# Kernel tuning notes

Measured on AMD Instinct MI355X. Metric: run time of the kernel, lower is better.

## Reference

```python
import jax, jax.numpy as jnp
import numpy as np

B = 32          # batch (decoding sequences)
HID = 4096      # hidden_size
NH = 32         # num query heads
NKV = 8         # num kv heads
HS = 128        # head_size
BS = 16         # paged-cache block size
MAXS = 2048     # max context length
MAXB = MAXS // BS            # blocks per sequence
NBLOCKS = B * MAXB           # total cache blocks
ROPE_BASE = 10000.0


def rope(x, pos):
    # NeoX rotate-half RoPE (offset = head_size//2, rotary_ndims = head_size).
    # x: [T, n_head, HS], pos: [T] int
    half = x.shape[-1] // 2
    inv_freq = 1.0 / (ROPE_BASE ** (jnp.arange(half, dtype=jnp.float32) * 2.0 / (2 * half)))
    freqs = pos[:, None].astype(jnp.float32) * inv_freq[None, :]   # [T, half]
    cos = jnp.cos(freqs)[:, None, :]
    sin = jnp.sin(freqs)[:, None, :]
    x1, x2 = x[..., :half], x[..., half:]
    return jnp.concatenate([x1 * cos - x2 * sin, x2 * cos + x1 * sin], axis=-1)


def setup_inputs() -> dict:
    key = jax.random.key(0)
    ks = jax.random.split(key, 8)
    hidden_states = jax.random.normal(ks[0], (B, 1, HID), jnp.float32)
    wq = jax.random.normal(ks[1], (NH * HS, HID), jnp.float32) * 0.02
    wk = jax.random.normal(ks[2], (NKV * HS, HID), jnp.float32) * 0.02
    wv = jax.random.normal(ks[3], (NKV * HS, HID), jnp.float32) * 0.02
    wo = jax.random.normal(ks[4], (NH * HS, NH * HS), jnp.float32) * 0.02
    k_cache = jax.random.normal(ks[5], (NBLOCKS, BS, NKV, HS), jnp.float32)
    v_cache = jax.random.normal(ks[6], (NBLOCKS, BS, NKV, HS), jnp.float32)
    # each sequence owns a disjoint set of MAXB blocks
    block_tables = jnp.arange(NBLOCKS, dtype=jnp.int32).reshape(B, MAXB)
    input_lengths = jax.random.randint(ks[7], (B,), 1, MAXS + 1, jnp.int32)
    position_ids = (input_lengths - 1).astype(jnp.int64)  # decode: write at last position
    last = input_lengths - 1
    slots = (block_tables[jnp.arange(B), last // BS] * BS + last % BS).astype(jnp.int32)
    return {
        "hidden_states": hidden_states, "wq": wq, "wk": wk, "wv": wv, "wo": wo,
        "k_cache": k_cache, "v_cache": v_cache, "position_ids": position_ids,
        "block_tables": block_tables, "slots": slots,
        "input_lengths": input_lengths, "max_s": MAXS,
    }


def reference(hidden_states, wq, wk, wv, wo, k_cache, v_cache,
              position_ids, block_tables, slots, input_lengths, max_s):
    bsz, q_len, hid = hidden_states.shape
    x = hidden_states.reshape(bsz * q_len, hid)
    q = (x @ wq.T).reshape(-1, NH, HS)
    k = (x @ wk.T).reshape(-1, NKV, HS)
    v = (x @ wv.T).reshape(-1, NKV, HS)
    q = rope(q, position_ids)
    k = rope(k, position_ids)
    # reshape_and_cache: scatter rope'd k and v into paged cache at slot indices
    kc = k_cache.reshape(-1, NKV, HS).at[slots].set(k)   # [NBLOCKS*BS, NKV, HS]
    vc = v_cache.reshape(-1, NKV, HS).at[slots].set(v)
    # single-query paged attention: gather per-sequence K/V via block_tables
    flat_idx = (block_tables[:, :, None] * BS
                + jnp.arange(BS, dtype=block_tables.dtype)[None, None, :]).reshape(bsz, -1)  # [B, max_s]
    keys = kc[flat_idx]    # [B, S, NKV, HS]
    vals = vc[flat_idx]    # [B, S, NKV, HS]
    groups = NH // NKV
    qg = q.reshape(bsz, NKV, groups, HS)
    scale = HS ** -0.5
    scores = jnp.einsum('bhgd,bshd->bhgs', qg, keys) * scale       # [B, NKV, G, S]
    valid = jnp.arange(max_s)[None, :] < input_lengths[:, None]    # [B, S]
    scores = jnp.where(valid[:, None, None, :], scores, -jnp.inf)
    p = jax.nn.softmax(scores, axis=-1)
    attn = jnp.einsum('bhgs,bshd->bhgd', p, vals).reshape(bsz, NH * HS)
    return (attn @ wo.T).reshape(bsz, q_len, hid)
```

## Files before the change

### kernel.cpp

```cpp
#include <hip/hip_runtime.h>
#include <math.h>


__device__ __forceinline__ void gemm_body(
    const float* __restrict__ x, const float* __restrict__ w,
    float* __restrict__ dst, int dstride, int kbase, int kcnt)
{
    __shared__ float xs[32][36];
    __shared__ float wsm[32][257];
    int t = threadIdx.x;
    float acc[4][8];
#pragma unroll
    for (int i = 0; i < 4; ++i)
#pragma unroll
        for (int j = 0; j < 8; ++j) acc[i][j] = 0.f;

    int nsub = t & 31, bsub = t >> 5;

    for (int kt = 0; kt < kcnt; kt += 32) {
        int k0 = kbase + kt;
        {
            int b = t >> 3, k4 = (t & 7) << 2;
            float4 xv = *(const float4*)(x + (size_t)b * 4096 + k0 + k4);
            *(float4*)&xs[b][k4] = xv;
        }
        {
            int k4 = (t & 7) << 2;
            int nl0 = t >> 3;
#pragma unroll
            for (int i = 0; i < 8; ++i) {
                int nl = nl0 + (i << 5);
                float4 wv = *(const float4*)(w + (size_t)nl * 4096 + k0 + k4);
                wsm[k4 + 0][nl] = wv.x;
                wsm[k4 + 1][nl] = wv.y;
                wsm[k4 + 2][nl] = wv.z;
                wsm[k4 + 3][nl] = wv.w;
            }
        }
        __syncthreads();
#pragma unroll
        for (int k = 0; k < 32; ++k) {
            float xv[4], wv[8];
#pragma unroll
            for (int j = 0; j < 4; ++j) xv[j] = xs[bsub * 4 + j][k];
#pragma unroll
            for (int j = 0; j < 8; ++j) wv[j] = wsm[k][nsub + (j << 5)];
#pragma unroll
            for (int jb = 0; jb < 4; ++jb)
#pragma unroll
                for (int jn = 0; jn < 8; ++jn)
                    acc[jb][jn] = fmaf(xv[jb], wv[jn], acc[jb][jn]);
        }
        __syncthreads();
    }
#pragma unroll
    for (int jb = 0; jb < 4; ++jb) {
        int b = bsub * 4 + jb;
#pragma unroll
        for (int jn = 0; jn < 8; ++jn)
            atomicAdd(dst + (size_t)b * dstride + nsub + (jn << 5), acc[jb][jn]);
    }
}

__global__ __launch_bounds__(256) void qkv_gemm(
    const float* __restrict__ x, const float* __restrict__ wq,
    const float* __restrict__ wk, const float* __restrict__ wv,
    float* __restrict__ qb, float* __restrict__ knb, float* __restrict__ vnb)
{
    int split = blockIdx.x & 15;
    int tile  = blockIdx.x >> 4;
    const float* w; float* dst; int dstride;
    if (tile < 16)      { w = wq + (size_t)tile * 256 * 4096;        dst = qb  + tile * 256;        dstride = 4096; }
    else if (tile < 20) { w = wk + (size_t)(tile - 16) * 256 * 4096; dst = knb + (tile - 16) * 256; dstride = 1024; }
    else                { w = wv + (size_t)(tile - 20) * 256 * 4096; dst = vnb + (tile - 20) * 256; dstride = 1024; }
    gemm_body(x, w, dst, dstride, split * 256, 256);
}

__global__ __launch_bounds__(256) void wo_gemm(
    const float* __restrict__ attn, const float* __restrict__ wo,
    float* __restrict__ out)
{
    int split = blockIdx.x & 15;
    int tile  = blockIdx.x >> 4;
    gemm_body(attn, wo + (size_t)tile * 256 * 4096, out + tile * 256, 4096, split * 256, 256);
}

__global__ void rope_kernel(float* __restrict__ qb, float* __restrict__ knb,
                            const int* __restrict__ lens)
{
    int bid = blockIdx.x;
    int b = bid / 40, r = bid % 40;
    float* row = (r < 32) ? (qb + (size_t)b * 4096 + r * 128)
                          : (knb + (size_t)b * 1024 + (r - 32) * 128);
    int d = threadIdx.x;
    float pos = (float)(lens[b] - 1);
    float inv = exp2f(-(float)d * 0.207620505930460f);
    float fr = pos * inv;
    float s, c;
    sincosf(fr, &s, &c);
    float x1 = row[d], x2 = row[d + 64];
    row[d]      = x1 * c - x2 * s;
    row[d + 64] = x2 * c + x1 * s;
}

#define MUL4(V, S) { V.x *= S; V.y *= S; V.z *= S; V.w *= S; }
#define FMA4(O, P, V) { O.x = fmaf(P, V.x, O.x); O.y = fmaf(P, V.y, O.y); \
                        O.z = fmaf(P, V.z, O.z); O.w = fmaf(P, V.w, O.w); }
#define DOT8(S, QA, QB, K0, K1) { \
    S = fmaf(QA.x, K0.x, S); S = fmaf(QA.y, K0.y, S); \
    S = fmaf(QA.z, K0.z, S); S = fmaf(QA.w, K0.w, S); \
    S = fmaf(QB.x, K1.x, S); S = fmaf(QB.y, K1.y, S); \
    S = fmaf(QB.z, K1.z, S); S = fmaf(QB.w, K1.w, S); }
#define RED16(X) { X += __shfl_xor(X, 1, 64); X += __shfl_xor(X, 2, 64); \
                   X += __shfl_xor(X, 4, 64); X += __shfl_xor(X, 8, 64); }
#define REDG_SUM(X) { X += __shfl_xor(X, 16, 64); X += __shfl_xor(X, 32, 64); }
#define REDG_MAX(X) { X = fmaxf(X, __shfl_xor(X, 16, 64)); \
                      X = fmaxf(X, __shfl_xor(X, 32, 64)); }
#define REDG_SUM4(V) { REDG_SUM(V.x) REDG_SUM(V.y) REDG_SUM(V.z) REDG_SUM(V.w) }

#define ALOADR(S, r_) { \
    int sl = ss[((r_) << 2) + g]; \
    const float* kp; const float* vp; \
    if (sl < 0) { kp = knew; vp = vnew; } \
    else { kp = kc + (size_t)sl * 1024 + hoff; vp = vc + (size_t)sl * 1024 + hoff; } \
    S##k0 = *(const float4*)(kp + isl); S##k1 = *(const float4*)(kp + isl + 4); \
    S##v0 = *(const float4*)(vp + isl); S##v1 = *(const float4*)(vp + isl + 4); }

#define OUPD(s_, m_, l_, Oa_, Ob_, V0_, V1_, vld_) { \
    if (s_ > m_) { \
        float c_ = __expf(m_ - s_); \
        l_ *= c_; MUL4(Oa_, c_) MUL4(Ob_, c_) \
        m_ = s_; \
    } \
    float pe_ = vld_ ? __expf(s_ - m_) : 0.f; \
    l_ += pe_; \
    FMA4(Oa_, pe_, V0_) FMA4(Ob_, pe_, V1_) }

#define ACOMP(S, r_) { \
    float s0 = 0.f, s1 = 0.f, s2 = 0.f, s3 = 0.f; \
    DOT8(s0, q0a, q0b, S##k0, S##k1) \
    DOT8(s1, q1a, q1b, S##k0, S##k1) \
    DOT8(s2, q2a, q2b, S##k0, S##k1) \
    DOT8(s3, q3a, q3b, S##k0, S##k1) \
    RED16(s0) RED16(s1) RED16(s2) RED16(s3) \
    int vld = (((r_) << 2) + g) < pend; \
    if (!vld) { s0 = s1 = s2 = s3 = -INFINITY; } \
    OUPD(s0, m0, l0, o0a, o0b, S##v0, S##v1, vld) \
    OUPD(s1, m1, l1, o1a, o1b, S##v0, S##v1, vld) \
    OUPD(s2, m2, l2, o2a, o2b, S##v0, S##v1, vld) \
    OUPD(s3, m3, l3, o3a, o3b, S##v0, S##v1, vld) }

__global__ __launch_bounds__(64, 1) void attn_kernel(
    const float* __restrict__ kc, const float* __restrict__ vc,
    const float* __restrict__ qb, const float* __restrict__ knb,
    const float* __restrict__ vnb,
    const int* __restrict__ btab, const int* __restrict__ lens,
    float* __restrict__ part)
{
    int bid = blockIdx.x;
    int c = bid & 15, h = (bid >> 4) & 7, b = bid >> 7;
    int len = lens[b];
    int p0 = c << 7;
    if (p0 >= len) return;
    int pend = min(len - p0, 128);
    int nr = (pend + 3) >> 2;
    int last = len - 1;

    __shared__ int ss[128];

    int lane = threadIdx.x;
    int g = lane >> 4;
    int isl = (lane & 15) << 3;
    int hoff = h * 128;

    {
        int idx = lane << 1;
        int p = p0 + idx;
        int bt = btab[b * 128 + (p >> 4)];
        int base = bt * 16 + (p & 15);
        ss[idx]     = (p     == last) ? -1 : base;
        ss[idx + 1] = (p + 1 == last) ? -1 : base + 1;
    }

    const float* knew = knb + ((size_t)b * 8 + h) * 128;
    const float* vnew = vnb + ((size_t)b * 8 + h) * 128;

    const float scale = 0.08838834764831845f;
    const float* qrow = qb + (size_t)b * 4096 + (size_t)h * 512;
    float4 q0a = *(const float4*)(qrow + isl),       q0b = *(const float4*)(qrow + isl + 4);
    float4 q1a = *(const float4*)(qrow + 128 + isl), q1b = *(const float4*)(qrow + 128 + isl + 4);
    float4 q2a = *(const float4*)(qrow + 256 + isl), q2b = *(const float4*)(qrow + 256 + isl + 4);
    float4 q3a = *(const float4*)(qrow + 384 + isl), q3b = *(const float4*)(qrow + 384 + isl + 4);
    MUL4(q0a, scale) MUL4(q0b, scale) MUL4(q1a, scale) MUL4(q1b, scale)
    MUL4(q2a, scale) MUL4(q2b, scale) MUL4(q3a, scale) MUL4(q3b, scale)

    float m0 = -INFINITY, m1 = -INFINITY, m2 = -INFINITY, m3 = -INFINITY;
    float l0 = 0.f, l1 = 0.f, l2 = 0.f, l3 = 0.f;
    float4 o0a = {0,0,0,0}, o0b = {0,0,0,0}, o1a = {0,0,0,0}, o1b = {0,0,0,0};
    float4 o2a = {0,0,0,0}, o2b = {0,0,0,0}, o3a = {0,0,0,0}, o3b = {0,0,0,0};

    float4 ak0, ak1, av0, av1;
    float4 bk0, bk1, bv0, bv1;
    float4 ck0, ck1, cv0, cv1;
    ALOADR(a, 0)
    if (1 < nr) ALOADR(b, 1)
    if (2 < nr) ALOADR(c, 2)
    for (int r = 0; r < nr; r += 3) {
        ACOMP(a, r)
        if (r + 3 < nr) ALOADR(a, r + 3)
        if (r + 1 >= nr) break;
        ACOMP(b, r + 1)
        if (r + 4 < nr) ALOADR(b, r + 4)
        if (r + 2 >= nr) break;
        ACOMP(c, r + 2)
        if (r + 5 < nr) ALOADR(c, r + 5)
    }

    float M0 = m0, M1 = m1, M2 = m2, M3 = m3;
    REDG_MAX(M0) REDG_MAX(M1) REDG_MAX(M2) REDG_MAX(M3)
    float w0 = __expf(m0 - M0), w1 = __expf(m1 - M1);
    float w2 = __expf(m2 - M2), w3 = __expf(m3 - M3);
    float L0 = w0 * l0, L1 = w1 * l1, L2 = w2 * l2, L3 = w3 * l3;
    REDG_SUM(L0) REDG_SUM(L1) REDG_SUM(L2) REDG_SUM(L3)
    MUL4(o0a, w0) MUL4(o0b, w0) MUL4(o1a, w1) MUL4(o1b, w1)
    MUL4(o2a, w2) MUL4(o2b, w2) MUL4(o3a, w3) MUL4(o3b, w3)
    REDG_SUM4(o0a) REDG_SUM4(o0b) REDG_SUM4(o1a) REDG_SUM4(o1b)
    REDG_SUM4(o2a) REDG_SUM4(o2b) REDG_SUM4(o3a) REDG_SUM4(o3b)

    float* pgb = part + (size_t)(((b * 8 + h) * 16 + c) * 4) * 132;
    if (lane < 16) {
        *(float4*)(pgb +       isl) = o0a; *(float4*)(pgb +       isl + 4) = o0b;
        *(float4*)(pgb + 132 + isl) = o1a; *(float4*)(pgb + 132 + isl + 4) = o1b;
        *(float4*)(pgb + 264 + isl) = o2a; *(float4*)(pgb + 264 + isl + 4) = o2b;
        *(float4*)(pgb + 396 + isl) = o3a; *(float4*)(pgb + 396 + isl + 4) = o3b;
    }
    if (lane == 0) {
        pgb[128] = M0; pgb[129] = L0;
        pgb[260] = M1; pgb[261] = L1;
        pgb[392] = M2; pgb[393] = L2;
        pgb[524] = M3; pgb[525] = L3;
    }
}

__global__ __launch_bounds__(256) void combine_kernel(
    const float* __restrict__ part, const int* __restrict__ lens,
    float* __restrict__ attn)
{
    int b = blockIdx.x >> 3, h = blockIdx.x & 7;
    int t = threadIdx.x;
    int g = t >> 6, lane = t & 63;
    int len = lens[b];
    int nch = (len + 127) >> 7;
    const float* base = part + (size_t)(b * 8 + h) * 8448 + (size_t)g * 132;
    float M = -INFINITY;
    for (int cc = 0; cc < nch; ++cc)
        M = fmaxf(M, base[(size_t)cc * 528 + 128]);
    float denom = 0.f, a0 = 0.f, a1 = 0.f;
    int d0 = lane << 1;
    for (int cc = 0; cc < nch; ++cc) {
        const float* pg = base + (size_t)cc * 528;
        float w = __expf(pg[128] - M);
        denom += w * pg[129];
        a0 += w * pg[d0];
        a1 += w * pg[d0 + 1];
    }
    float inv = 1.f / denom;
    float* dst = attn + (size_t)b * 4096 + (size_t)(h * 4 + g) * 128 + d0;
    dst[0] = a0 * inv;
    dst[1] = a1 * inv;
}

extern "C" void kernel_launch(void* const* d_in, const int* in_sizes, int n_in,
                              void* d_out, int out_size, void* d_ws, size_t ws_size,
                              hipStream_t stream)
{
    const float* x   = (const float*)d_in[0];
    const float* wq  = (const float*)d_in[1];
    const float* wk  = (const float*)d_in[2];
    const float* wv  = (const float*)d_in[3];
    const float* wo  = (const float*)d_in[4];
    const float* kc  = (const float*)d_in[5];
    const float* vc  = (const float*)d_in[6];
    const int* btab  = (const int*)d_in[8];
    const int* lens  = (const int*)d_in[10];

    float* qb   = (float*)d_ws;
    float* knb  = qb  + 32 * 4096;
    float* vnb  = knb + 32 * 1024;
    float* attn = vnb + 32 * 1024;
    float* part = attn + 32 * 4096;
    float* outp = (float*)d_out;

    hipMemsetAsync(d_ws, 0, (size_t)(32 * 4096 + 2 * 32 * 1024) * sizeof(float), stream);
    hipMemsetAsync(d_out, 0, (size_t)32 * 4096 * sizeof(float), stream);

    qkv_gemm<<<24 * 16, 256, 0, stream>>>(x, wq, wk, wv, qb, knb, vnb);
    rope_kernel<<<32 * 40, 64, 0, stream>>>(qb, knb, lens);
    attn_kernel<<<4096, 64, 0, stream>>>(kc, vc, qb, knb, vnb, btab, lens, part);
    combine_kernel<<<256, 256, 0, stream>>>(part, lens, attn);
    wo_gemm<<<16 * 16, 256, 0, stream>>>(attn, wo, outp);
}
```

Before: 178.1 us.

## Remap attention so each wave covers all KV heads over 32-token chunks

Restructures the paged attention kernel so a 64-lane wave handles one batch and a 32-token chunk across all 8 KV heads. Each 8-lane group owns one head, and each lane holds 16 contiguous dims. Every token row of the K/V cache is therefore read as one contiguous 4 KB span instead of 512-byte per-head slices. The change also drops the shared-memory slot table and the cross-group softmax reduction, and shortens the shuffle reduction to 8 lanes. In exchange the kernel uses more registers per lane, has no inner validity masking, and produces four times more partial chunks for the combine kernel to merge.

After: 199.0 us. +11.7%, slower.

```diff
diff --git a/kernel.cpp b/kernel.cpp
--- a/kernel.cpp
+++ b/kernel.cpp
@@ -103,52 +103,50 @@
     row[d + 64] = x2 * c + x1 * s;
 }
 
-#define MUL4(V, S) { V.x *= S; V.y *= S; V.z *= S; V.w *= S; }
-#define FMA4(O, P, V) { O.x = fmaf(P, V.x, O.x); O.y = fmaf(P, V.y, O.y); \
-                        O.z = fmaf(P, V.z, O.z); O.w = fmaf(P, V.w, O.w); }
-#define DOT8(S, QA, QB, K0, K1) { \
-    S = fmaf(QA.x, K0.x, S); S = fmaf(QA.y, K0.y, S); \
-    S = fmaf(QA.z, K0.z, S); S = fmaf(QA.w, K0.w, S); \
-    S = fmaf(QB.x, K1.x, S); S = fmaf(QB.y, K1.y, S); \
-    S = fmaf(QB.z, K1.z, S); S = fmaf(QB.w, K1.w, S); }
-#define RED16(X) { X += __shfl_xor(X, 1, 64); X += __shfl_xor(X, 2, 64); \
-                   X += __shfl_xor(X, 4, 64); X += __shfl_xor(X, 8, 64); }
-#define REDG_SUM(X) { X += __shfl_xor(X, 16, 64); X += __shfl_xor(X, 32, 64); }
-#define REDG_MAX(X) { X = fmaxf(X, __shfl_xor(X, 16, 64)); \
-                      X = fmaxf(X, __shfl_xor(X, 32, 64)); }
-#define REDG_SUM4(V) { REDG_SUM(V.x) REDG_SUM(V.y) REDG_SUM(V.z) REDG_SUM(V.w) }
-
-#define ALOADR(S, r_) { \
-    int sl = ss[((r_) << 2) + g]; \
-    const float* kp; const float* vp; \
-    if (sl < 0) { kp = knew; vp = vnew; } \
-    else { kp = kc + (size_t)sl * 1024 + hoff; vp = vc + (size_t)sl * 1024 + hoff; } \
-    S##k0 = *(const float4*)(kp + isl); S##k1 = *(const float4*)(kp + isl + 4); \
-    S##v0 = *(const float4*)(vp + isl); S##v1 = *(const float4*)(vp + isl + 4); }
-
-#define OUPD(s_, m_, l_, Oa_, Ob_, V0_, V1_, vld_) { \
+#define V4MUL(V, S) { V.x *= S; V.y *= S; V.z *= S; V.w *= S; }
+#define V4FMA(O, P, V) { O.x = fmaf(P, V.x, O.x); O.y = fmaf(P, V.y, O.y); \
+                         O.z = fmaf(P, V.z, O.z); O.w = fmaf(P, V.w, O.w); }
+#define DOT4(S, Q, K) { S = fmaf(Q.x, K.x, S); S = fmaf(Q.y, K.y, S); \
+                        S = fmaf(Q.z, K.z, S); S = fmaf(Q.w, K.w, S); }
+#define RED8(X) { X += __shfl_xor(X, 1, 64); X += __shfl_xor(X, 2, 64); \
+                  X += __shfl_xor(X, 4, 64); }
+
+#define LOADR(S, r_) { \
+    int p_ = p0 + (r_); \
+    const float* kp_; const float* vp_; \
+    if (p_ == last) { kp_ = knew; vp_ = vnew; } \
+    else { \
+        int sl_ = ((r_) < 16) ? (bt0x16 + (r_)) : (bt1x16 + (r_) - 16); \
+        kp_ = kc + (size_t)sl_ * 1024 + l16; \
+        vp_ = vc + (size_t)sl_ * 1024 + l16; \
+    } \
+    S##k0 = *(const float4*)(kp_);      S##k1 = *(const float4*)(kp_ + 4); \
+    S##k2 = *(const float4*)(kp_ + 8);  S##k3 = *(const float4*)(kp_ + 12); \
+    S##v0 = *(const float4*)(vp_);      S##v1 = *(const float4*)(vp_ + 4); \
+    S##v2 = *(const float4*)(vp_ + 8);  S##v3 = *(const float4*)(vp_ + 12); }
+
+#define OUPD(S, s_, m_, l_, O0_, O1_, O2_, O3_) { \
     if (s_ > m_) { \
         float c_ = __expf(m_ - s_); \
-        l_ *= c_; MUL4(Oa_, c_) MUL4(Ob_, c_) \
+        l_ *= c_; V4MUL(O0_, c_) V4MUL(O1_, c_) V4MUL(O2_, c_) V4MUL(O3_, c_) \
         m_ = s_; \
     } \
-    float pe_ = vld_ ? __expf(s_ - m_) : 0.f; \
+    float pe_ = __expf(s_ - m_); \
     l_ += pe_; \
-    FMA4(Oa_, pe_, V0_) FMA4(Ob_, pe_, V1_) }
-
-#define ACOMP(S, r_) { \
+    V4FMA(O0_, pe_, S##v0) V4FMA(O1_, pe_, S##v1) \
+    V4FMA(O2_, pe_, S##v2) V4FMA(O3_, pe_, S##v3) }
+
+#define COMP(S, r_) { \
     float s0 = 0.f, s1 = 0.f, s2 = 0.f, s3 = 0.f; \
-    DOT8(s0, q0a, q0b, S##k0, S##k1) \
-    DOT8(s1, q1a, q1b, S##k0, S##k1) \
-    DOT8(s2, q2a, q2b, S##k0, S##k1) \
-    DOT8(s3, q3a, q3b, S##k0, S##k1) \
-    RED16(s0) RED16(s1) RED16(s2) RED16(s3) \
-    int vld = (((r_) << 2) + g) < pend; \
-    if (!vld) { s0 = s1 = s2 = s3 = -INFINITY; } \
-    OUPD(s0, m0, l0, o0a, o0b, S##v0, S##v1, vld) \
-    OUPD(s1, m1, l1, o1a, o1b, S##v0, S##v1, vld) \
-    OUPD(s2, m2, l2, o2a, o2b, S##v0, S##v1, vld) \
-    OUPD(s3, m3, l3, o3a, o3b, S##v0, S##v1, vld) }
+    DOT4(s0, q00, S##k0) DOT4(s0, q01, S##k1) DOT4(s0, q02, S##k2) DOT4(s0, q03, S##k3) \
+    DOT4(s1, q10, S##k0) DOT4(s1, q11, S##k1) DOT4(s1, q12, S##k2) DOT4(s1, q13, S##k3) \
+    DOT4(s2, q20, S##k0) DOT4(s2, q21, S##k1) DOT4(s2, q22, S##k2) DOT4(s2, q23, S##k3) \
+    DOT4(s3, q30, S##k0) DOT4(s3, q31, S##k1) DOT4(s3, q32, S##k2) DOT4(s3, q33, S##k3) \
+    RED8(s0) RED8(s1) RED8(s2) RED8(s3) \
+    OUPD(S, s0, m0, l0, o00, o01, o02, o03) \
+    OUPD(S, s1, m1, l1, o10, o11, o12, o13) \
+    OUPD(S, s2, m2, l2, o20, o21, o22, o23) \
+    OUPD(S, s3, m3, l3, o30, o31, o32, o33) }
 
 __global__ __launch_bounds__(64, 1) void attn_kernel(
     const float* __restrict__ kc, const float* __restrict__ vc,
@@ -158,87 +156,74 @@
     float* __restrict__ part)
 {
     int bid = blockIdx.x;
-    int c = bid & 15, h = (bid >> 4) & 7, b = bid >> 7;
+    int c = bid >> 5, b = bid & 31;
     int len = lens[b];
-    int p0 = c << 7;
+    int p0 = c << 5;
     if (p0 >= len) return;
-    int pend = min(len - p0, 128);
-    int nr = (pend + 3) >> 2;
+    int pend = min(len - p0, 32);
     int last = len - 1;
 
-    __shared__ int ss[128];
-
     int lane = threadIdx.x;
-    int g = lane >> 4;
-    int isl = (lane & 15) << 3;
-    int hoff = h * 128;
-
-    {
-        int idx = lane << 1;
-        int p = p0 + idx;
-        int bt = btab[b * 128 + (p >> 4)];
-        int base = bt * 16 + (p & 15);
-        ss[idx]     = (p     == last) ? -1 : base;
-        ss[idx + 1] = (p + 1 == last) ? -1 : base + 1;
-    }
-
-    const float* knew = knb + ((size_t)b * 8 + h) * 128;
-    const float* vnew = vnb + ((size_t)b * 8 + h) * 128;
+    int h = lane >> 3;
+    int i = lane & 7;
+    int l16 = lane << 4;
+
+    int bt0x16 = btab[b * 128 + (p0 >> 4)] << 4;
+    int bt1x16 = btab[b * 128 + (p0 >> 4) + 1] << 4;
+
+    const float* knew = knb + (size_t)b * 1024 + l16;
+    const float* vnew = vnb + (size_t)b * 1024 + l16;
 
     const float scale = 0.08838834764831845f;
-    const float* qrow = qb + (size_t)b * 4096 + (size_t)h * 512;
-    float4 q0a = *(const float4*)(qrow + isl),       q0b = *(const float4*)(qrow + isl + 4);
-    float4 q1a = *(const float4*)(qrow + 128 + isl), q1b = *(const float4*)(qrow + 128 + isl + 4);
-    float4 q2a = *(const float4*)(qrow + 256 + isl), q2b = *(const float4*)(qrow + 256 + isl + 4);
-    float4 q3a = *(const float4*)(qrow + 384 + isl), q3b = *(const float4*)(qrow + 384 + isl + 4);
-    MUL4(q0a, scale) MUL4(q0b, scale) MUL4(q1a, scale) MUL4(q1b, scale)
-    MUL4(q2a, scale) MUL4(q2b, scale) MUL4(q3a, scale) MUL4(q3b, scale)
+    const float* qr = qb + (size_t)b * 4096 + (size_t)h * 512 + (i << 4);
+    float4 q00 = *(const float4*)(qr),        q01 = *(const float4*)(qr + 4);
+    float4 q02 = *(const float4*)(qr + 8),    q03 = *(const float4*)(qr + 12);
+    float4 q10 = *(const float4*)(qr + 128),  q11 = *(const float4*)(qr + 132);
+    float4 q12 = *(const float4*)(qr + 136),  q13 = *(const float4*)(qr + 140);
+    float4 q20 = *(const float4*)(qr + 256),  q21 = *(const float4*)(qr + 260);
+    float4 q22 = *(const float4*)(qr + 264),  q23 = *(const float4*)(qr + 268);
+    float4 q30 = *(const float4*)(qr + 384),  q31 = *(const float4*)(qr + 388);
+    float4 q32 = *(const float4*)(qr + 392),  q33 = *(const float4*)(qr + 396);
+    V4MUL(q00, scale) V4MUL(q01, scale) V4MUL(q02, scale) V4MUL(q03, scale)
+    V4MUL(q10, scale) V4MUL(q11, scale) V4MUL(q12, scale) V4MUL(q13, scale)
+    V4MUL(q20, scale) V4MUL(q21, scale) V4MUL(q22, scale) V4MUL(q23, scale)
+    V4MUL(q30, scale) V4MUL(q31, scale) V4MUL(q32, scale) V4MUL(q33, scale)
 
     float m0 = -INFINITY, m1 = -INFINITY, m2 = -INFINITY, m3 = -INFINITY;
     float l0 = 0.f, l1 = 0.f, l2 = 0.f, l3 = 0.f;
-    float4 o0a = {0,0,0,0}, o0b = {0,0,0,0}, o1a = {0,0,0,0}, o1b = {0,0,0,0};
-    float4 o2a = {0,0,0,0}, o2b = {0,0,0,0}, o3a = {0,0,0,0}, o3b = {0,0,0,0};
-
-    float4 ak0, ak1, av0, av1;
-    float4 bk0, bk1, bv0, bv1;
-    float4 ck0, ck1, cv0, cv1;
-    ALOADR(a, 0)
-    if (1 < nr) ALOADR(b, 1)
-    if (2 < nr) ALOADR(c, 2)
-    for (int r = 0; r < nr; r += 3) {
-        ACOMP(a, r)
-        if (r + 3 < nr) ALOADR(a, r + 3)
-        if (r + 1 >= nr) break;
-        ACOMP(b, r + 1)
-        if (r + 4 < nr) ALOADR(b, r + 4)
-        if (r + 2 >= nr) break;
-        ACOMP(c, r + 2)
-        if (r + 5 < nr) ALOADR(c, r + 5)
-    }
-
-    float M0 = m0, M1 = m1, M2 = m2, M3 = m3;
-    REDG_MAX(M0) REDG_MAX(M1) REDG_MAX(M2) REDG_MAX(M3)
-    float w0 = __expf(m0 - M0), w1 = __expf(m1 - M1);
-    float w2 = __expf(m2 - M2), w3 = __expf(m3 - M3);
-    float L0 = w0 * l0, L1 = w1 * l1, L2 = w2 * l2, L3 = w3 * l3;
-    REDG_SUM(L0) REDG_SUM(L1) REDG_SUM(L2) REDG_SUM(L3)
-    MUL4(o0a, w0) MUL4(o0b, w0) MUL4(o1a, w1) MUL4(o1b, w1)
-    MUL4(o2a, w2) MUL4(o2b, w2) MUL4(o3a, w3) MUL4(o3b, w3)
-    REDG_SUM4(o0a) REDG_SUM4(o0b) REDG_SUM4(o1a) REDG_SUM4(o1b)
-    REDG_SUM4(o2a) REDG_SUM4(o2b) REDG_SUM4(o3a) REDG_SUM4(o3b)
-
-    float* pgb = part + (size_t)(((b * 8 + h) * 16 + c) * 4) * 132;
-    if (lane < 16) {
-        *(float4*)(pgb +       isl) = o0a; *(float4*)(pgb +       isl + 4) = o0b;
-        *(float4*)(pgb + 132 + isl) = o1a; *(float4*)(pgb + 132 + isl + 4) = o1b;
-        *(float4*)(pgb + 264 + isl) = o2a; *(float4*)(pgb + 264 + isl + 4) = o2b;
-        *(float4*)(pgb + 396 + isl) = o3a; *(float4*)(pgb + 396 + isl + 4) = o3b;
-    }
-    if (lane == 0) {
-        pgb[128] = M0; pgb[129] = L0;
-        pgb[260] = M1; pgb[261] = L1;
-        pgb[392] = M2; pgb[393] = L2;
-        pgb[524] = M3; pgb[525] = L3;
+    float4 o00 = {0,0,0,0}, o01 = {0,0,0,0}, o02 = {0,0,0,0}, o03 = {0,0,0,0};
+    float4 o10 = {0,0,0,0}, o11 = {0,0,0,0}, o12 = {0,0,0,0}, o13 = {0,0,0,0};
+    float4 o20 = {0,0,0,0}, o21 = {0,0,0,0}, o22 = {0,0,0,0}, o23 = {0,0,0,0};
+    float4 o30 = {0,0,0,0}, o31 = {0,0,0,0}, o32 = {0,0,0,0}, o33 = {0,0,0,0};
+
+    float4 ak0, ak1, ak2, ak3, av0, av1, av2, av3;
+    float4 bk0, bk1, bk2, bk3, bv0, bv1, bv2, bv3;
+
+    LOADR(a, 0)
+    if (1 < pend) LOADR(b, 1)
+    for (int r = 0; r < pend; r += 2) {
+        COMP(a, r)
+        if (r + 2 < pend) LOADR(a, r + 2)
+        if (r + 1 >= pend) break;
+        COMP(b, r + 1)
+        if (r + 3 < pend) LOADR(b, r + 3)
+    }
+
+    float* pgb = part + (size_t)(b * 64 + c) * 4224;
+    int i16 = i << 4;
+    float* d0 = pgb + (size_t)(h * 4 + 0) * 132 + i16;
+    float* d1 = pgb + (size_t)(h * 4 + 1) * 132 + i16;
+    float* d2 = pgb + (size_t)(h * 4 + 2) * 132 + i16;
+    float* d3 = pgb + (size_t)(h * 4 + 3) * 132 + i16;
+    *(float4*)(d0) = o00; *(float4*)(d0 + 4) = o01; *(float4*)(d0 + 8) = o02; *(float4*)(d0 + 12) = o03;
+    *(float4*)(d1) = o10; *(float4*)(d1 + 4) = o11; *(float4*)(d1 + 8) = o12; *(float4*)(d1 + 12) = o13;
+    *(float4*)(d2) = o20; *(float4*)(d2 + 4) = o21; *(float4*)(d2 + 8) = o22; *(float4*)(d2 + 12) = o23;
+    *(float4*)(d3) = o30; *(float4*)(d3 + 4) = o31; *(float4*)(d3 + 8) = o32; *(float4*)(d3 + 12) = o33;
+    if (i == 0) {
+        pgb[(h * 4 + 0) * 132 + 128] = m0; pgb[(h * 4 + 0) * 132 + 129] = l0;
+        pgb[(h * 4 + 1) * 132 + 128] = m1; pgb[(h * 4 + 1) * 132 + 129] = l1;
+        pgb[(h * 4 + 2) * 132 + 128] = m2; pgb[(h * 4 + 2) * 132 + 129] = l2;
+        pgb[(h * 4 + 3) * 132 + 128] = m3; pgb[(h * 4 + 3) * 132 + 129] = l3;
     }
 }
 
@@ -250,15 +235,15 @@
     int t = threadIdx.x;
     int g = t >> 6, lane = t & 63;
     int len = lens[b];
-    int nch = (len + 127) >> 7;
-    const float* base = part + (size_t)(b * 8 + h) * 8448 + (size_t)g * 132;
+    int nch = (len + 31) >> 5;
+    const float* base = part + (size_t)b * 64 * 4224 + (size_t)(h * 4 + g) * 132;
     float M = -INFINITY;
     for (int cc = 0; cc < nch; ++cc)
-        M = fmaxf(M, base[(size_t)cc * 528 + 128]);
+        M = fmaxf(M, base[(size_t)cc * 4224 + 128]);
     float denom = 0.f, a0 = 0.f, a1 = 0.f;
     int d0 = lane << 1;
     for (int cc = 0; cc < nch; ++cc) {
-        const float* pg = base + (size_t)cc * 528;
+        const float* pg = base + (size_t)cc * 4224;
         float w = __expf(pg[128] - M);
         denom += w * pg[129];
         a0 += w * pg[d0];
@@ -296,7 +281,7 @@
 
     qkv_gemm<<<24 * 16, 256, 0, stream>>>(x, wq, wk, wv, qb, knb, vnb);
     rope_kernel<<<32 * 40, 64, 0, stream>>>(qb, knb, lens);
-    attn_kernel<<<4096, 64, 0, stream>>>(kc, vc, qb, knb, vnb, btab, lens, part);
+    attn_kernel<<<2048, 64, 0, stream>>>(kc, vc, qb, knb, vnb, btab, lens, part);
     combine_kernel<<<256, 256, 0, stream>>>(part, lens, attn);
     wo_gemm<<<16 * 16, 256, 0, stream>>>(attn, wo, outp);
 }
```

## Replace fp32 tiled GEMMs with bf16 MFMA split-K kernels for QKV and output projections

Applied to the files above, without the earlier changes.

Rewrites the QKV and output projection GEMMs to use 16x16x32 bf16 MFMA instructions, converting fp32 activations and weights to bf16 in registers. Each wave computes a 16x16 output tile over a quarter of K, loading directly from global memory without shared-memory staging, and accumulates with atomics. This aims to cut the FMA instruction cost, but it reads each weight row once per 16-row batch half and reduces input precision to bf16.

New measurement: 181.5 us. About the same (+1.9%).

```diff
diff --git a/kernel.cpp b/kernel.cpp
--- a/kernel.cpp
+++ b/kernel.cpp
@@ -2,87 +2,80 @@
 #include <math.h>
 
 
-__device__ __forceinline__ void gemm_body(
-    const float* __restrict__ x, const float* __restrict__ w,
-    float* __restrict__ dst, int dstride, int kbase, int kcnt)
-{
-    __shared__ float xs[32][36];
-    __shared__ float wsm[32][257];
-    int t = threadIdx.x;
-    float acc[4][8];
-#pragma unroll
-    for (int i = 0; i < 4; ++i)
-#pragma unroll
-        for (int j = 0; j < 8; ++j) acc[i][j] = 0.f;
-
-    int nsub = t & 31, bsub = t >> 5;
-
-    for (int kt = 0; kt < kcnt; kt += 32) {
-        int k0 = kbase + kt;
-        {
-            int b = t >> 3, k4 = (t & 7) << 2;
-            float4 xv = *(const float4*)(x + (size_t)b * 4096 + k0 + k4);
-            *(float4*)&xs[b][k4] = xv;
-        }
-        {
-            int k4 = (t & 7) << 2;
-            int nl0 = t >> 3;
-#pragma unroll
-            for (int i = 0; i < 8; ++i) {
-                int nl = nl0 + (i << 5);
-                float4 wv = *(const float4*)(w + (size_t)nl * 4096 + k0 + k4);
-                wsm[k4 + 0][nl] = wv.x;
-                wsm[k4 + 1][nl] = wv.y;
-                wsm[k4 + 2][nl] = wv.z;
-                wsm[k4 + 3][nl] = wv.w;
-            }
-        }
-        __syncthreads();
-#pragma unroll
-        for (int k = 0; k < 32; ++k) {
-            float xv[4], wv[8];
-#pragma unroll
-            for (int j = 0; j < 4; ++j) xv[j] = xs[bsub * 4 + j][k];
-#pragma unroll
-            for (int j = 0; j < 8; ++j) wv[j] = wsm[k][nsub + (j << 5)];
-#pragma unroll
-            for (int jb = 0; jb < 4; ++jb)
-#pragma unroll
-                for (int jn = 0; jn < 8; ++jn)
-                    acc[jb][jn] = fmaf(xv[jb], wv[jn], acc[jb][jn]);
-        }
-        __syncthreads();
-    }
-#pragma unroll
-    for (int jb = 0; jb < 4; ++jb) {
-        int b = bsub * 4 + jb;
-#pragma unroll
-        for (int jn = 0; jn < 8; ++jn)
-            atomicAdd(dst + (size_t)b * dstride + nsub + (jn << 5), acc[jb][jn]);
-    }
-}
-
-__global__ __launch_bounds__(256) void qkv_gemm(
+typedef __attribute__((ext_vector_type(8))) short bf16x8;
+typedef __attribute__((ext_vector_type(4))) float f32x4;
+
+__device__ __forceinline__ unsigned short f2bf(float f) {
+    unsigned int u = __float_as_uint(f);
+    return (unsigned short)((u + 0x7FFFu + ((u >> 16) & 1u)) >> 16);
+}
+__device__ __forceinline__ bf16x8 cvt8(float4 a, float4 b) {
+    bf16x8 r;
+    r[0] = (short)f2bf(a.x); r[1] = (short)f2bf(a.y);
+    r[2] = (short)f2bf(a.z); r[3] = (short)f2bf(a.w);
+    r[4] = (short)f2bf(b.x); r[5] = (short)f2bf(b.y);
+    r[6] = (short)f2bf(b.z); r[7] = (short)f2bf(b.w);
+    return r;
+}
+
+__device__ __forceinline__ void mfma_tile(
+    const float* __restrict__ xp, const float* __restrict__ wp,
+    float* __restrict__ dst, int dstr, int n0, int mh, int lane)
+{
+    f32x4 acc = {0.f, 0.f, 0.f, 0.f};
+#pragma unroll 4
+    for (int s = 0; s < 32; ++s) {
+        float4 xa = *(const float4*)(xp + s * 32);
+        float4 xb = *(const float4*)(xp + s * 32 + 4);
+        float4 wa = *(const float4*)(wp + s * 32);
+        float4 wb = *(const float4*)(wp + s * 32 + 4);
+        acc = __builtin_amdgcn_mfma_f32_16x16x32_bf16(
+            cvt8(xa, xb), cvt8(wa, wb), acc, 0, 0, 0);
+    }
+    int ccol = n0 + (lane & 15);
+    int rbase = mh * 16 + ((lane >> 4) << 2);
+    atomicAdd(dst + (size_t)(rbase + 0) * dstr + ccol, acc[0]);
+    atomicAdd(dst + (size_t)(rbase + 1) * dstr + ccol, acc[1]);
+    atomicAdd(dst + (size_t)(rbase + 2) * dstr + ccol, acc[2]);
+    atomicAdd(dst + (size_t)(rbase + 3) * dstr + ccol, acc[3]);
+}
+
+__global__ __launch_bounds__(256) void qkv_mfma(
     const float* __restrict__ x, const float* __restrict__ wq,
     const float* __restrict__ wk, const float* __restrict__ wv,
     float* __restrict__ qb, float* __restrict__ knb, float* __restrict__ vnb)
 {
-    int split = blockIdx.x & 15;
-    int tile  = blockIdx.x >> 4;
-    const float* w; float* dst; int dstride;
-    if (tile < 16)      { w = wq + (size_t)tile * 256 * 4096;        dst = qb  + tile * 256;        dstride = 4096; }
-    else if (tile < 20) { w = wk + (size_t)(tile - 16) * 256 * 4096; dst = knb + (tile - 16) * 256; dstride = 1024; }
-    else                { w = wv + (size_t)(tile - 20) * 256 * 4096; dst = vnb + (tile - 20) * 256; dstride = 1024; }
-    gemm_body(x, w, dst, dstride, split * 256, 256);
-}
-
-__global__ __launch_bounds__(256) void wo_gemm(
+    int gw = (blockIdx.x << 2) + (threadIdx.x >> 6);
+    int lane = threadIdx.x & 63;
+    int split = gw & 3;
+    int mh = (gw >> 2) & 1;
+    int nt = gw >> 3;
+    const float* w; float* dst; int dstr; int n0;
+    if (nt < 256)      { w = wq; n0 = nt * 16;         dst = qb;  dstr = 4096; }
+    else if (nt < 320) { w = wk; n0 = (nt - 256) * 16; dst = knb; dstr = 1024; }
+    else               { w = wv; n0 = (nt - 320) * 16; dst = vnb; dstr = 1024; }
+    int row = lane & 15, kq = (lane >> 4) << 3;
+    int kbase = split << 10;
+    const float* xp = x + (size_t)(mh * 16 + row) * 4096 + kbase + kq;
+    const float* wp = w + (size_t)(n0 + row) * 4096 + kbase + kq;
+    mfma_tile(xp, wp, dst, dstr, n0, mh, lane);
+}
+
+__global__ __launch_bounds__(256) void wo_mfma(
     const float* __restrict__ attn, const float* __restrict__ wo,
     float* __restrict__ out)
 {
-    int split = blockIdx.x & 15;
-    int tile  = blockIdx.x >> 4;
-    gemm_body(attn, wo + (size_t)tile * 256 * 4096, out + tile * 256, 4096, split * 256, 256);
+    int gw = (blockIdx.x << 2) + (threadIdx.x >> 6);
+    int lane = threadIdx.x & 63;
+    int split = gw & 3;
+    int mh = (gw >> 2) & 1;
+    int nt = gw >> 3;
+    int n0 = nt * 16;
+    int row = lane & 15, kq = (lane >> 4) << 3;
+    int kbase = split << 10;
+    const float* xp = attn + (size_t)(mh * 16 + row) * 4096 + kbase + kq;
+    const float* wp = wo + (size_t)(n0 + row) * 4096 + kbase + kq;
+    mfma_tile(xp, wp, out, 4096, n0, mh, lane);
 }
 
 __global__ void rope_kernel(float* __restrict__ qb, float* __restrict__ knb,
@@ -294,9 +287,9 @@
     hipMemsetAsync(d_ws, 0, (size_t)(32 * 4096 + 2 * 32 * 1024) * sizeof(float), stream);
     hipMemsetAsync(d_out, 0, (size_t)32 * 4096 * sizeof(float), stream);
 
-    qkv_gemm<<<24 * 16, 256, 0, stream>>>(x, wq, wk, wv, qb, knb, vnb);
+    qkv_mfma<<<768, 256, 0, stream>>>(x, wq, wk, wv, qb, knb, vnb);
     rope_kernel<<<32 * 40, 64, 0, stream>>>(qb, knb, lens);
     attn_kernel<<<4096, 64, 0, stream>>>(kc, vc, qb, knb, vnb, btab, lens, part);
     combine_kernel<<<256, 256, 0, stream>>>(part, lens, attn);
-    wo_gemm<<<16 * 16, 256, 0, stream>>>(attn, wo, outp);
-}
+    wo_mfma<<<512, 256, 0, stream>>>(attn, wo, outp);
+}
```
